# Performance work log

Measured on AMD Instinct MI355X. Metric: run time of the kernel, lower is better.

The kernel has to match this reference:

```python
import jax, jax.numpy as jnp
import numpy as np

B, T, D = 2, 2048, 2048
H, HKV = 16, 16
SEM, GEO = 1024, 1024
DH = D // H          # 128, v head dim
DS = SEM // H        # 64, sem head dim
DG = GEO // H        # 64, geo head dim (== rope_dim)
ROPE_BASE = 10000.0


def _split_heads(x, n_heads, hd):
    b, t, _ = x.shape
    return x.reshape(b, t, n_heads, hd).transpose(0, 2, 1, 3)  # (B,H,T,hd)


def _rope(x, pos_offset):
    # x: (B,H,T,DG); rotate-half RoPE over the full geo head dim
    b, h, t, d = x.shape
    inv_freq = 1.0 / (ROPE_BASE ** (jnp.arange(0, d, 2, dtype=jnp.float32) / d))
    pos = jnp.arange(t, dtype=jnp.float32) + jnp.float32(pos_offset)
    ang = pos[:, None] * inv_freq[None, :]            # (T, d/2)
    cos, sin = jnp.cos(ang), jnp.sin(ang)             # (T, d/2)
    x1, x2 = x[..., : d // 2], x[..., d // 2 :]
    return jnp.concatenate([x1 * cos - x2 * sin, x2 * cos + x1 * sin], axis=-1)


def setup_inputs() -> dict:
    key = jax.random.key(0)
    ks = jax.random.split(key, 8)
    s = lambda fan_in: 1.0 / np.sqrt(fan_in)
    return {
        "x": jax.random.normal(ks[0], (B, T, D), dtype=jnp.float32),
        "Wq_sem": jax.random.normal(ks[1], (D, SEM), dtype=jnp.float32) * s(D),
        "Wk_sem": jax.random.normal(ks[2], (D, SEM), dtype=jnp.float32) * s(D),
        "Wq_geo": jax.random.normal(ks[3], (D, GEO), dtype=jnp.float32) * s(D),
        "Wk_geo": jax.random.normal(ks[4], (D, GEO), dtype=jnp.float32) * s(D),
        "Wv": jax.random.normal(ks[5], (D, D), dtype=jnp.float32) * s(D),
        "Wo": jax.random.normal(ks[6], (D, D), dtype=jnp.float32) * s(D),
        "gate_logit": jax.random.normal(ks[7], (H,), dtype=jnp.float32) * 0.1,
        "pos_offset": 0,
    }


def reference(x, Wq_sem, Wk_sem, Wq_geo, Wk_geo, Wv, Wo, gate_logit, pos_offset):
    qsh = _split_heads(x @ Wq_sem, H, DS)    # (B,H,T,DS)
    ksh = _split_heads(x @ Wk_sem, HKV, DS)
    qgh = _split_heads(x @ Wq_geo, H, DG)    # (B,H,T,DG)
    kgh = _split_heads(x @ Wk_geo, HKV, DG)
    vh = _split_heads(x @ Wv, HKV, DH)       # (B,H,T,DH)

    qgh = _rope(qgh, pos_offset)
    kgh = _rope(kgh, pos_offset)

    gate = jax.nn.sigmoid(gate_logit).reshape(1, H, 1, 1).astype(x.dtype)
    qsh = qsh * (2.0 * gate)
    qgh = qgh * (2.0 - 2.0 * gate)

    sem_scale = 1.0 / np.sqrt(float(DS))
    geo_scale = 1.0 / np.sqrt(float(DG))
    # decoupled logits: sem and geo contributions each with their own scale
    logits = (jnp.einsum("bhqd,bhkd->bhqk", qsh, ksh) * sem_scale
              + jnp.einsum("bhqd,bhkd->bhqk", qgh, kgh) * geo_scale)

    t = x.shape[1]
    causal = jnp.tril(jnp.ones((t, t), dtype=bool))
    logits = jnp.where(causal, logits, jnp.finfo(logits.dtype).min)
    attn = jax.nn.softmax(logits, axis=-1)

    out_h = jnp.einsum("bhqk,bhkd->bhqd", attn, vh)   # (B,H,T,DH)
    out = out_h.transpose(0, 2, 1, 3).reshape(x.shape[0], t, H * DH)
    return out @ Wo
```

## Files before the change

### kernel.cpp

```cpp
#include <hip/hip_runtime.h>
#include <hip/hip_bf16.h>
#include <math.h>

#define B_ 2
#define T_ 2048
#define D_ 2048
#define H_ 16
#define DH_ 128
#define SEM_ 1024
#define GEO_ 1024
#define NPROJ 6144

typedef unsigned short ushort_t;
typedef short bf16x8 __attribute__((ext_vector_type(8)));
typedef float f32x4 __attribute__((ext_vector_type(4)));

static __device__ inline ushort_t f2b(float x) {
    __hip_bfloat16 h = __float2bfloat16(x);
    return *reinterpret_cast<ushort_t*>(&h);
}
static __device__ inline float b2f(ushort_t u) {
    union { unsigned int i; float f; } v; v.i = ((unsigned int)u) << 16; return v.f;
}
static __device__ inline void gload_lds16(const ushort_t* g, ushort_t* l) {
    __builtin_amdgcn_global_load_lds(
        (const __attribute__((address_space(1))) void*)g,
        (__attribute__((address_space(3))) void*)l, 16, 0, 0);
}

__global__ __launch_bounds__(256) void convert_x(
    const float* __restrict__ x, ushort_t* __restrict__ xh)
{
    size_t i = ((size_t)blockIdx.x * 256 + threadIdx.x) * 8;
    float4 a = *(const float4*)&x[i];
    float4 b = *(const float4*)&x[i + 4];
    bf16x8 o;
    o[0] = (short)f2b(a.x); o[1] = (short)f2b(a.y);
    o[2] = (short)f2b(a.z); o[3] = (short)f2b(a.w);
    o[4] = (short)f2b(b.x); o[5] = (short)f2b(b.y);
    o[6] = (short)f2b(b.z); o[7] = (short)f2b(b.w);
    *(bf16x8*)&xh[i] = o;
}

__global__ __launch_bounds__(256) void transpose_all(
    const float* __restrict__ W0, const float* __restrict__ W1,
    const float* __restrict__ W2, const float* __restrict__ W3,
    const float* __restrict__ W4, const float* __restrict__ W5,
    ushort_t* __restrict__ Wt_all, ushort_t* __restrict__ WoT)
{
    const int z = blockIdx.z;
    const float* W;
    ushort_t* dst;
    int N;
    switch (z) {
        case 0: W = W0; dst = Wt_all;                          N = 1024; break;
        case 1: W = W1; dst = Wt_all + (size_t)1024 * 2048;    N = 1024; break;
        case 2: W = W2; dst = Wt_all + (size_t)2048 * 2048;    N = 1024; break;
        case 3: W = W3; dst = Wt_all + (size_t)3072 * 2048;    N = 1024; break;
        case 4: W = W4; dst = Wt_all + (size_t)4096 * 2048;    N = 2048; break;
        default: W = W5; dst = WoT;                            N = 2048; break;
    }
    const int n0 = blockIdx.x * 32;
    if (n0 >= N) return;
    const int k0 = blockIdx.y * 32;

    __shared__ float tile[32][33];
    const int c = threadIdx.x & 31, r = threadIdx.x >> 5;
#pragma unroll
    for (int rr = 0; rr < 32; rr += 8)
        tile[r + rr][c] = W[(size_t)(k0 + r + rr) * N + n0 + c];
    __syncthreads();
#pragma unroll
    for (int rr = 0; rr < 32; rr += 8)
        dst[(size_t)(n0 + r + rr) * 2048 + k0 + c] = f2b(tile[c][r + rr]);
}

__global__ __launch_bounds__(256) void gemm_proj(
    const ushort_t* __restrict__ A, const ushort_t* __restrict__ Bt,
    const float* __restrict__ gate_logit, const int* __restrict__ pos_off,
    ushort_t* __restrict__ Qh, ushort_t* __restrict__ Kh,
    ushort_t* __restrict__ Vt)
{
    const int K = 2048;
    __shared__ ushort_t As[128 * 32];
    __shared__ ushort_t Bs[128 * 32];

    const int tid  = threadIdx.x;
    const int wid  = tid >> 6, lane = tid & 63;
    const int ln16 = lane & 15, g = lane >> 4;
    const int wm = wid & 1, wn = wid >> 1;
    const int m0 = blockIdx.y * 128, n0 = blockIdx.x * 128;

    const int lrow = lane >> 2;
    const int lc8  = (lane & 3) * 8;
    const ushort_t* gA = A  + (size_t)(m0 + wid * 32 + lrow) * K + lc8;
    const ushort_t* gB = Bt + (size_t)(n0 + wid * 32 + lrow) * K + lc8;
    ushort_t* lA = As + wid * 1024;
    ushort_t* lB = Bs + wid * 1024;
    const size_t K16 = (size_t)16 * K;

    f32x4 acc[4][4];
#pragma unroll
    for (int i = 0; i < 4; ++i)
#pragma unroll
        for (int j = 0; j < 4; ++j) acc[i][j] = (f32x4){0.f, 0.f, 0.f, 0.f};

    for (int k0 = 0; k0 < K; k0 += 32) {
        __syncthreads();
        gload_lds16(gA,       lA);
        gload_lds16(gA + K16, lA + 512);
        gload_lds16(gB,       lB);
        gload_lds16(gB + K16, lB + 512);
        gA += 32; gB += 32;
        __syncthreads();

        bf16x8 af[4], bfr[4];
#pragma unroll
        for (int i = 0; i < 4; ++i)
            af[i] = *(const bf16x8*)&As[(wm * 64 + i * 16 + ln16) * 32 + g * 8];
#pragma unroll
        for (int j = 0; j < 4; ++j)
            bfr[j] = *(const bf16x8*)&Bs[(wn * 64 + j * 16 + ln16) * 32 + g * 8];
#pragma unroll
        for (int i = 0; i < 4; ++i)
#pragma unroll
            for (int j = 0; j < 4; ++j)
                acc[i][j] = __builtin_amdgcn_mfma_f32_16x16x32_bf16(
                    af[i], bfr[j], acc[i][j], 0, 0, 0);
    }

    const int region = n0 >> 10;
    const int rbase  = m0 + wm * 64 + g * 4;

    if (region <= 1) {
        const int h = ((n0 & 1023) >> 6) + wn;
        ushort_t* dst = (region == 0) ? Qh : Kh;
        float sc = 1.0f;
        if (region == 0) {
            float sg = 1.0f / (1.0f + __expf(-gate_logit[h]));
            sc = 0.25f * sg;
        }
#pragma unroll
        for (int i = 0; i < 4; ++i)
#pragma unroll
            for (int r = 0; r < 4; ++r) {
                int row = rbase + i * 16 + r;
                int t = row & (T_ - 1), bb = row >> 11;
                size_t base = ((size_t)(bb * H_ + h) * T_ + t) * 128;
#pragma unroll
                for (int j = 0; j < 4; ++j)
                    dst[base + j * 16 + ln16] = f2b(acc[i][j][r] * sc);
            }
    } else if (region <= 3) {
        const int h = ((n0 & 1023) >> 6) + wn;
        ushort_t* dst = (region == 2) ? Qh : Kh;
        float sc = 1.0f;
        if (region == 2) {
            float sg = 1.0f / (1.0f + __expf(-gate_logit[h]));
            sc = 0.25f * (1.0f - sg);
        }
        const float po = (float)(*pos_off);
#pragma unroll
        for (int j = 0; j < 2; ++j) {
            const int ip = j * 16 + ln16;
            const float invf = __expf(-0.28782313665087625f * (float)ip);
#pragma unroll
            for (int i = 0; i < 4; ++i)
#pragma unroll
                for (int r = 0; r < 4; ++r) {
                    int row = rbase + i * 16 + r;
                    int t = row & (T_ - 1), bb = row >> 11;
                    float s, c;
                    __sincosf(((float)t + po) * invf, &s, &c);
                    float x1 = acc[i][j][r], x2 = acc[i][j + 2][r];
                    size_t base = ((size_t)(bb * H_ + h) * T_ + t) * 128;
                    dst[base + 64 + ip] = f2b((x1 * c - x2 * s) * sc);
                    dst[base + 96 + ip] = f2b((x2 * c + x1 * s) * sc);
                }
        }
    } else {
        const int h = (n0 - 4096) >> 7;
#pragma unroll
        for (int j = 0; j < 4; ++j) {
            const int d = wn * 64 + j * 16 + ln16;
            size_t dbase = ((size_t)((n0 >= 4096 ? 0 : 0) ) ); (void)dbase;
#pragma unroll
            for (int i = 0; i < 4; ++i)
#pragma unroll
                for (int r = 0; r < 4; ++r) {
                    int row = rbase + i * 16 + r;
                    int t = row & (T_ - 1), bb = row >> 11;
                    Vt[((size_t)(bb * H_ + h) * DH_ + d) * T_ + t] =
                        f2b(acc[i][j][r]);
                }
        }
    }
}

__global__ __launch_bounds__(256) void gemm_bt_f32(
    const ushort_t* __restrict__ A, const ushort_t* __restrict__ Bt,
    float* __restrict__ C, int M, int N, int K)
{
    __shared__ ushort_t As[128 * 32];
    __shared__ ushort_t Bs[128 * 32];

    const int tid  = threadIdx.x;
    const int wid  = tid >> 6, lane = tid & 63;
    const int ln16 = lane & 15, g = lane >> 4;
    const int wm = wid & 1, wn = wid >> 1;
    const int m0 = blockIdx.y * 128, n0 = blockIdx.x * 128;

    const int lrow = lane >> 2;
    const int lc8  = (lane & 3) * 8;
    const ushort_t* gA = A  + (size_t)(m0 + wid * 32 + lrow) * K + lc8;
    const ushort_t* gB = Bt + (size_t)(n0 + wid * 32 + lrow) * K + lc8;
    ushort_t* lA = As + wid * 1024;
    ushort_t* lB = Bs + wid * 1024;
    const size_t K16 = (size_t)16 * K;

    f32x4 acc[4][4];
#pragma unroll
    for (int i = 0; i < 4; ++i)
#pragma unroll
        for (int j = 0; j < 4; ++j) acc[i][j] = (f32x4){0.f, 0.f, 0.f, 0.f};

    for (int k0 = 0; k0 < K; k0 += 32) {
        __syncthreads();
        gload_lds16(gA,       lA);
        gload_lds16(gA + K16, lA + 512);
        gload_lds16(gB,       lB);
        gload_lds16(gB + K16, lB + 512);
        gA += 32; gB += 32;
        __syncthreads();

        bf16x8 af[4], bfr[4];
#pragma unroll
        for (int i = 0; i < 4; ++i)
            af[i] = *(const bf16x8*)&As[(wm * 64 + i * 16 + ln16) * 32 + g * 8];
#pragma unroll
        for (int j = 0; j < 4; ++j)
            bfr[j] = *(const bf16x8*)&Bs[(wn * 64 + j * 16 + ln16) * 32 + g * 8];
#pragma unroll
        for (int i = 0; i < 4; ++i)
#pragma unroll
            for (int j = 0; j < 4; ++j)
                acc[i][j] = __builtin_amdgcn_mfma_f32_16x16x32_bf16(
                    af[i], bfr[j], acc[i][j], 0, 0, 0);
    }

#pragma unroll
    for (int i = 0; i < 4; ++i)
#pragma unroll
        for (int j = 0; j < 4; ++j)
#pragma unroll
            for (int r = 0; r < 4; ++r) {
                int row = m0 + wm * 64 + i * 16 + g * 4 + r;
                int col = n0 + wn * 64 + j * 16 + ln16;
                C[(size_t)row * N + col] = acc[i][j][r];
            }
}

#define P_PITCH  40

__global__ __launch_bounds__(256) void flash_attn(
    const ushort_t* __restrict__ Qh,
    const ushort_t* __restrict__ Kh,
    const ushort_t* __restrict__ Vt,
    ushort_t* __restrict__ aoh)
{
    __shared__ ushort_t Ks[32 * 128];
    __shared__ ushort_t Vs[128 * 32];
    __shared__ ushort_t Pl[4 * 16 * P_PITCH];

    const int tid  = threadIdx.x;
    const int wid  = tid >> 6, lane = tid & 63;
    const int ln16 = lane & 15, g = lane >> 4;
    const int p    = blockIdx.x;
    const int h  = blockIdx.y, b = blockIdx.z;
    const int bh = b * H_ + h;

    const ushort_t* Kbase = Kh + (size_t)bh * T_ * 128;
    const ushort_t* Vbase = Vt + (size_t)bh * 128 * T_;
    ushort_t* Pw = Pl + wid * 16 * P_PITCH;

    const int sk0 = tid,      sk1 = 256 + tid;
    const int kr0 = sk0 >> 4, kc0 = sk0 & 15;
    const int kr1 = sk1 >> 4, kc1 = sk1 & 15;
    const int vd0 = sk0 >> 2, vg0 = sk0 & 3;
    const int vd1 = sk1 >> 2, vg1 = sk1 & 3;
    const int kofs0 = (kc0 ^ (kr0 & 15)) * 8, kofs1 = (kc1 ^ (kr1 & 15)) * 8;
    const int vofs0 = (vg0 ^ ((vd0 + (vd0 >> 2)) & 3)) * 8;
    const int vofs1 = (vg1 ^ ((vd1 + (vd1 >> 2)) & 3)) * 8;

    bf16x8 bones;
    {
        short o = (ln16 == 0) ? (short)0x3F80 : (short)0;
#pragma unroll
        for (int j = 0; j < 8; ++j) bones[j] = o;
    }

#pragma unroll 1
    for (int ti = 0; ti < 2; ++ti) {
        const int qt = ti ? (31 - p) : p;
        const int q0 = qt * 64;
        const int qw = q0 + wid * 16;

        bf16x8 aq[4];
        {
            const ushort_t* qrow = Qh + ((size_t)bh * T_ + qw + ln16) * 128;
#pragma unroll
            for (int c2 = 0; c2 < 4; ++c2)
                aq[c2] = *(const bf16x8*)(qrow + c2 * 32 + g * 8);
        }

        f32x4 acc[8];
#pragma unroll
        for (int i = 0; i < 8; ++i) acc[i] = (f32x4){0.f, 0.f, 0.f, 0.f};
        f32x4 acc_l = (f32x4){0.f, 0.f, 0.f, 0.f};

        const int nkb  = q0 / 32 + 2;
        const int qmax = qw + 15;

        for (int kb = 0; kb < nkb; ++kb) {
            const int kt = kb * 32;
            __syncthreads();
            gload_lds16(Kbase + (size_t)(kt + kr0) * 128 + kofs0, Ks + wid * 512);
            gload_lds16(Kbase + (size_t)(kt + kr1) * 128 + kofs1, Ks + 2048 + wid * 512);
            gload_lds16(Vbase + (size_t)vd0 * T_ + kt + vofs0,    Vs + wid * 512);
            gload_lds16(Vbase + (size_t)vd1 * T_ + kt + vofs1,    Vs + 2048 + wid * 512);
            __syncthreads();
            if (kt > qmax) continue;

            f32x4 s0 = (f32x4){0.f, 0.f, 0.f, 0.f};
            f32x4 s1 = (f32x4){0.f, 0.f, 0.f, 0.f};
#pragma unroll
            for (int c2 = 0; c2 < 4; ++c2) {
                int jk = c2 * 4 + g;
                bf16x8 bk0 = *(const bf16x8*)&Ks[(ln16 * 16 + (jk ^ ln16)) * 8];
                bf16x8 bk1 = *(const bf16x8*)&Ks[(256 + ln16 * 16 + (jk ^ ln16)) * 8];
                s0 = __builtin_amdgcn_mfma_f32_16x16x32_bf16(aq[c2], bk0, s0, 0, 0, 0);
                s1 = __builtin_amdgcn_mfma_f32_16x16x32_bf16(aq[c2], bk1, s1, 0, 0, 0);
            }

            const bool diag = (kt + 31 > qw);
#pragma unroll
            for (int r2 = 0; r2 < 4; ++r2) {
                float e0 = __expf(s0[r2] - 12.0f);
                float e1 = __expf(s1[r2] - 12.0f);
                if (diag) {
                    int qr = qw + g * 4 + r2;
                    e0 = (kt + ln16      > qr) ? 0.0f : e0;
                    e1 = (kt + 16 + ln16 > qr) ? 0.0f : e1;
                }
                int prow = g * 4 + r2;
                Pw[prow * P_PITCH + ln16]      = f2b(e0);
                Pw[prow * P_PITCH + 16 + ln16] = f2b(e1);
            }
            __asm__ volatile("s_waitcnt lgkmcnt(0)" ::: "memory");
            bf16x8 ap = *(const bf16x8*)&Pw[ln16 * P_PITCH + g * 8];

#pragma unroll
            for (int cdv = 0; cdv < 8; ++cdv) {
                int d = cdv * 16 + ln16;
                bf16x8 bv = *(const bf16x8*)
                    &Vs[((d << 2) + (g ^ ((d + (d >> 2)) & 3))) * 8];
                acc[cdv] = __builtin_amdgcn_mfma_f32_16x16x32_bf16(ap, bv, acc[cdv], 0, 0, 0);
            }
            acc_l = __builtin_amdgcn_mfma_f32_16x16x32_bf16(ap, bones, acc_l, 0, 0, 0);
        }

        float invl[4];
#pragma unroll
        for (int r2 = 0; r2 < 4; ++r2)
            invl[r2] = 1.0f / __shfl(acc_l[r2], lane & 48);
#pragma unroll
        for (int cdv = 0; cdv < 8; ++cdv)
#pragma unroll
            for (int r2 = 0; r2 < 4; ++r2) {
                int qr = qw + g * 4 + r2;
                aoh[((size_t)b * T_ + qr) * D_ + h * DH_ + cdv * 16 + ln16] =
                    f2b(acc[cdv][r2] * invl[r2]);
            }
    }
}

extern "C" void kernel_launch(void* const* d_in, const int* in_sizes, int n_in,
                              void* d_out, int out_size, void* d_ws, size_t ws_size,
                              hipStream_t stream)
{
    const float* x       = (const float*)d_in[0];
    const float* Wq_sem  = (const float*)d_in[1];
    const float* Wk_sem  = (const float*)d_in[2];
    const float* Wq_geo  = (const float*)d_in[3];
    const float* Wk_geo  = (const float*)d_in[4];
    const float* Wv      = (const float*)d_in[5];
    const float* Wo      = (const float*)d_in[6];
    const float* gate    = (const float*)d_in[7];
    const int*   pos_off = (const int*)d_in[8];
    float* out = (float*)d_out;

    const int M = B_ * T_;
    char* ws = (char*)d_ws;
    ushort_t* xh     = (ushort_t*)(ws);
    ushort_t* aoh    = xh;
    ushort_t* Wt_all = (ushort_t*)(ws + (size_t)16 * 1048576);
    ushort_t* WoT    = (ushort_t*)(ws + (size_t)40 * 1048576);
    ushort_t* Qh     = (ushort_t*)(ws + (size_t)48 * 1048576);
    ushort_t* Kh     = (ushort_t*)(ws + (size_t)64 * 1048576);
    ushort_t* Vt     = (ushort_t*)(ws + (size_t)80 * 1048576);

    dim3 blk(256);

    convert_x<<<(M * D_) / (256 * 8), blk, 0, stream>>>(x, xh);
    transpose_all<<<dim3(64, 64, 6), blk, 0, stream>>>(
        Wq_sem, Wk_sem, Wq_geo, Wk_geo, Wv, Wo, Wt_all, WoT);

    gemm_proj<<<dim3(NPROJ / 128, M / 128), blk, 0, stream>>>(
        xh, Wt_all, gate, pos_off, Qh, Kh, Vt);

    flash_attn<<<dim3(16, H_, B_), blk, 0, stream>>>(Qh, Kh, Vt, aoh);

    gemm_bt_f32<<<dim3(D_ / 128, M / 128), blk, 0, stream>>>(
        aoh, WoT, out, M, D_, D_);
}
```

Measured before the change: 420.5 us.

## Rewrite projection GEMM as 256x256 double-buffered pipelined MFMA kernel

Replaces the 128x128, 256-thread projection GEMM (which synchronized twice per 32-wide K step) with a 256x256 tile, 512-thread kernel using 128KB of dynamic LDS. It double-buffers 64-wide K tiles, interleaves async global-to-LDS staging of the next tile with quadrant-wise MFMA, swizzles LDS addresses, and raises wave priority around the MFMA blocks. The epilogue is remapped so each wave writes two heads with RoPE and gate scaling as before. This aims to hide load latency and raise MFMA utilization, at the cost of heavy register pressure, fewer blocks in the grid, and fragile hand-written waitcnt and barrier ordering.

```diff
diff --git a/kernel.cpp b/kernel.cpp
--- a/kernel.cpp
+++ b/kernel.cpp
@@ -75,125 +75,185 @@
         dst[(size_t)(n0 + r + rr) * 2048 + k0 + c] = f2b(tile[c][r + rr]);
 }
 
-__global__ __launch_bounds__(256) void gemm_proj(
+#define BARS()  { asm volatile("" ::: "memory"); __builtin_amdgcn_s_barrier(); asm volatile("" ::: "memory"); }
+#define WL0()   asm volatile("s_waitcnt lgkmcnt(0)" ::: "memory")
+#define WV6()   asm volatile("s_waitcnt vmcnt(6)" ::: "memory")
+
+#define LDA8(par, iq, i4, kk) \
+    (*(const bf16x8*)&smA[(par)*16384 + (iq)*8192 + aoff + (i4)*1024 + (kk)*32])
+#define LDB8(par, jq, j1, kk) \
+    (*(const bf16x8*)&smB[(par)*16384 + (jq)*8192 + boff + (j1)*2048 + (kk)*32])
+
+#define READ_A(par, iq) \
+    aF[0]=LDA8(par,iq,0,0); aF[1]=LDA8(par,iq,0,1); \
+    aF[2]=LDA8(par,iq,1,0); aF[3]=LDA8(par,iq,1,1); \
+    aF[4]=LDA8(par,iq,2,0); aF[5]=LDA8(par,iq,2,1); \
+    aF[6]=LDA8(par,iq,3,0); aF[7]=LDA8(par,iq,3,1);
+
+#define READ_B(par, jq) \
+    bF[(jq)*4+0]=LDB8(par,jq,0,0); bF[(jq)*4+1]=LDB8(par,jq,0,1); \
+    bF[(jq)*4+2]=LDB8(par,jq,1,0); bF[(jq)*4+3]=LDB8(par,jq,1,1);
+
+#define STAGE_A(h, kt, par) do { \
+    const ushort_t* _s = gAbase + (size_t)((h)*128) * 2048 + (kt)*64 + stgoff; \
+    ushort_t* _d = smA + (par)*16384 + (h)*8192 + wid*512; \
+    gload_lds16(_s, _d); \
+    gload_lds16(_s + (size_t)64*2048, _d + 4096); \
+} while(0)
+
+#define STAGE_B(h, kt, par) do { \
+    const ushort_t* _s = gBbase + (size_t)((h)*128) * 2048 + (kt)*64 + stgoff; \
+    ushort_t* _d = smB + (par)*16384 + (h)*8192 + wid*512; \
+    gload_lds16(_s, _d); \
+    gload_lds16(_s + (size_t)64*2048, _d + 4096); \
+} while(0)
+
+#define MM16(iq, jq) do { \
+    _Pragma("unroll") \
+    for (int i4 = 0; i4 < 4; ++i4) { \
+        acc[(iq)*4+i4][(jq)*2+0] = __builtin_amdgcn_mfma_f32_16x16x32_bf16(aF[i4*2+0], bF[(jq)*4+0], acc[(iq)*4+i4][(jq)*2+0], 0, 0, 0); \
+        acc[(iq)*4+i4][(jq)*2+0] = __builtin_amdgcn_mfma_f32_16x16x32_bf16(aF[i4*2+1], bF[(jq)*4+1], acc[(iq)*4+i4][(jq)*2+0], 0, 0, 0); \
+        acc[(iq)*4+i4][(jq)*2+1] = __builtin_amdgcn_mfma_f32_16x16x32_bf16(aF[i4*2+0], bF[(jq)*4+2], acc[(iq)*4+i4][(jq)*2+1], 0, 0, 0); \
+        acc[(iq)*4+i4][(jq)*2+1] = __builtin_amdgcn_mfma_f32_16x16x32_bf16(aF[i4*2+1], bF[(jq)*4+3], acc[(iq)*4+i4][(jq)*2+1], 0, 0, 0); \
+    } \
+} while(0)
+
+#define TILE_BODY(par, parn, kt1, kt2) \
+    READ_A(par, 0); READ_B(par, 0); STAGE_A(1, kt1, parn); \
+    BARS(); WL0(); \
+    __builtin_amdgcn_s_setprio(1); MM16(0, 0); __builtin_amdgcn_s_setprio(0); \
+    BARS(); \
+    READ_B(par, 1); STAGE_A(0, kt2, par); \
+    BARS(); WL0(); \
+    __builtin_amdgcn_s_setprio(1); MM16(0, 1); __builtin_amdgcn_s_setprio(0); \
+    BARS(); \
+    READ_A(par, 1); STAGE_B(0, kt2, par); \
+    BARS(); WL0(); \
+    __builtin_amdgcn_s_setprio(1); MM16(1, 1); __builtin_amdgcn_s_setprio(0); \
+    BARS(); \
+    STAGE_B(1, kt2, par); WV6(); \
+    BARS(); \
+    __builtin_amdgcn_s_setprio(1); MM16(1, 0); __builtin_amdgcn_s_setprio(0); \
+    BARS();
+
+__global__ __launch_bounds__(512, 2) void gemm_proj(
     const ushort_t* __restrict__ A, const ushort_t* __restrict__ Bt,
     const float* __restrict__ gate_logit, const int* __restrict__ pos_off,
     ushort_t* __restrict__ Qh, ushort_t* __restrict__ Kh,
     ushort_t* __restrict__ Vt)
 {
-    const int K = 2048;
-    __shared__ ushort_t As[128 * 32];
-    __shared__ ushort_t Bs[128 * 32];
+    extern __shared__ __align__(16) ushort_t smdyn[];
+    ushort_t* smA = smdyn;
+    ushort_t* smB = smdyn + 32768;
 
     const int tid  = threadIdx.x;
     const int wid  = tid >> 6, lane = tid & 63;
     const int ln16 = lane & 15, g = lane >> 4;
     const int wm = wid & 1, wn = wid >> 1;
-    const int m0 = blockIdx.y * 128, n0 = blockIdx.x * 128;
-
-    const int lrow = lane >> 2;
-    const int lc8  = (lane & 3) * 8;
-    const ushort_t* gA = A  + (size_t)(m0 + wid * 32 + lrow) * K + lc8;
-    const ushort_t* gB = Bt + (size_t)(n0 + wid * 32 + lrow) * K + lc8;
-    ushort_t* lA = As + wid * 1024;
-    ushort_t* lB = Bs + wid * 1024;
-    const size_t K16 = (size_t)16 * K;
-
-    f32x4 acc[4][4];
-#pragma unroll
-    for (int i = 0; i < 4; ++i)
+    const int m0 = blockIdx.y * 256, n0 = blockIdx.x * 256;
+
+    const int srow = wid * 8 + (lane >> 3);
+    const int scol = ((lane & 7) * 8) ^ ((lane & 32) ? 16 : 0);
+    const size_t stgoff = (size_t)srow * 2048 + scol;
+    const ushort_t* gAbase = A  + (size_t)m0 * 2048;
+    const ushort_t* gBbase = Bt + (size_t)n0 * 2048;
+
+    const int sw   = (ln16 & 4) << 2;
+    const int aoff = wm * 4096 + ln16 * 64 + ((g * 8) ^ sw);
+    const int boff = (wn >> 1) * 4096 + (wn & 1) * 1024 + ln16 * 64 + ((g * 8) ^ sw);
+
+    f32x4 acc[8][4];
+#pragma unroll
+    for (int i = 0; i < 8; ++i)
 #pragma unroll
         for (int j = 0; j < 4; ++j) acc[i][j] = (f32x4){0.f, 0.f, 0.f, 0.f};
-
-    for (int k0 = 0; k0 < K; k0 += 32) {
-        __syncthreads();
-        gload_lds16(gA,       lA);
-        gload_lds16(gA + K16, lA + 512);
-        gload_lds16(gB,       lB);
-        gload_lds16(gB + K16, lB + 512);
-        gA += 32; gB += 32;
-        __syncthreads();
-
-        bf16x8 af[4], bfr[4];
-#pragma unroll
-        for (int i = 0; i < 4; ++i)
-            af[i] = *(const bf16x8*)&As[(wm * 64 + i * 16 + ln16) * 32 + g * 8];
-#pragma unroll
-        for (int j = 0; j < 4; ++j)
-            bfr[j] = *(const bf16x8*)&Bs[(wn * 64 + j * 16 + ln16) * 32 + g * 8];
-#pragma unroll
-        for (int i = 0; i < 4; ++i)
-#pragma unroll
-            for (int j = 0; j < 4; ++j)
-                acc[i][j] = __builtin_amdgcn_mfma_f32_16x16x32_bf16(
-                    af[i], bfr[j], acc[i][j], 0, 0, 0);
-    }
+    bf16x8 aF[8], bF[8];
+
+    STAGE_A(0, 0, 0); STAGE_B(0, 0, 0); STAGE_B(1, 0, 0); STAGE_A(1, 0, 0);
+    STAGE_A(0, 1, 1); STAGE_B(0, 1, 1); STAGE_B(1, 1, 1);
+    WV6();
+    BARS();
+
+#pragma unroll 1
+    for (int t = 0; t < 32; t += 2) {
+        const int ka1 = t + 1;
+        const int ka2 = (t + 2 < 32) ? t + 2 : 31;
+        const int kb1 = ka2;
+        const int kb2 = (t + 3 < 32) ? t + 3 : 31;
+        TILE_BODY(0, 1, ka1, ka2);
+        TILE_BODY(1, 0, kb1, kb2);
+    }
+    asm volatile("s_waitcnt vmcnt(0)" ::: "memory");
 
     const int region = n0 >> 10;
     const int rbase  = m0 + wm * 64 + g * 4;
 
     if (region <= 1) {
-        const int h = ((n0 & 1023) >> 6) + wn;
         ushort_t* dst = (region == 0) ? Qh : Kh;
-        float sc = 1.0f;
+        const int hb  = ((n0 & 1023) >> 6) + (wn >> 1);
+        const int d64 = (wn & 1) * 16 + ln16;
+        float sc0 = 1.0f, sc1 = 1.0f;
         if (region == 0) {
-            float sg = 1.0f / (1.0f + __expf(-gate_logit[h]));
-            sc = 0.25f * sg;
+            sc0 = 0.25f / (1.0f + __expf(-gate_logit[hb]));
+            sc1 = 0.25f / (1.0f + __expf(-gate_logit[hb + 2]));
         }
 #pragma unroll
-        for (int i = 0; i < 4; ++i)
+        for (int i = 0; i < 8; ++i)
 #pragma unroll
             for (int r = 0; r < 4; ++r) {
-                int row = rbase + i * 16 + r;
+                int row = rbase + (i >> 2) * 128 + (i & 3) * 16 + r;
                 int t = row & (T_ - 1), bb = row >> 11;
-                size_t base = ((size_t)(bb * H_ + h) * T_ + t) * 128;
-#pragma unroll
-                for (int j = 0; j < 4; ++j)
-                    dst[base + j * 16 + ln16] = f2b(acc[i][j][r] * sc);
+                size_t b0 = ((size_t)(bb * H_ + hb)     * T_ + t) * 128;
+                size_t b1 = ((size_t)(bb * H_ + hb + 2) * T_ + t) * 128;
+                dst[b0 + d64]      = f2b(acc[i][0][r] * sc0);
+                dst[b0 + d64 + 32] = f2b(acc[i][1][r] * sc0);
+                dst[b1 + d64]      = f2b(acc[i][2][r] * sc1);
+                dst[b1 + d64 + 32] = f2b(acc[i][3][r] * sc1);
             }
     } else if (region <= 3) {
-        const int h = ((n0 & 1023) >> 6) + wn;
         ushort_t* dst = (region == 2) ? Qh : Kh;
-        float sc = 1.0f;
+        const int hb = ((n0 & 1023) >> 6) + (wn >> 1);
+        const int ip = (wn & 1) * 16 + ln16;
+        const float invf = __expf(-0.28782313665087625f * (float)ip);
+        const float po = (float)(*pos_off);
+        float sc0 = 1.0f, sc1 = 1.0f;
         if (region == 2) {
-            float sg = 1.0f / (1.0f + __expf(-gate_logit[h]));
-            sc = 0.25f * (1.0f - sg);
+            sc0 = 0.25f * (1.0f - 1.0f / (1.0f + __expf(-gate_logit[hb])));
+            sc1 = 0.25f * (1.0f - 1.0f / (1.0f + __expf(-gate_logit[hb + 2])));
         }
-        const float po = (float)(*pos_off);
-#pragma unroll
-        for (int j = 0; j < 2; ++j) {
-            const int ip = j * 16 + ln16;
-            const float invf = __expf(-0.28782313665087625f * (float)ip);
-#pragma unroll
-            for (int i = 0; i < 4; ++i)
-#pragma unroll
-                for (int r = 0; r < 4; ++r) {
-                    int row = rbase + i * 16 + r;
-                    int t = row & (T_ - 1), bb = row >> 11;
-                    float s, c;
-                    __sincosf(((float)t + po) * invf, &s, &c);
-                    float x1 = acc[i][j][r], x2 = acc[i][j + 2][r];
-                    size_t base = ((size_t)(bb * H_ + h) * T_ + t) * 128;
-                    dst[base + 64 + ip] = f2b((x1 * c - x2 * s) * sc);
-                    dst[base + 96 + ip] = f2b((x2 * c + x1 * s) * sc);
-                }
-        }
+#pragma unroll
+        for (int i = 0; i < 8; ++i)
+#pragma unroll
+            for (int r = 0; r < 4; ++r) {
+                int row = rbase + (i >> 2) * 128 + (i & 3) * 16 + r;
+                int t = row & (T_ - 1), bb = row >> 11;
+                float s, c;
+                __sincosf(((float)t + po) * invf, &s, &c);
+                size_t b0 = ((size_t)(bb * H_ + hb)     * T_ + t) * 128;
+                size_t b1 = ((size_t)(bb * H_ + hb + 2) * T_ + t) * 128;
+                float x1 = acc[i][0][r], x2 = acc[i][1][r];
+                dst[b0 + 64 + ip] = f2b((x1 * c - x2 * s) * sc0);
+                dst[b0 + 96 + ip] = f2b((x2 * c + x1 * s) * sc0);
+                x1 = acc[i][2][r]; x2 = acc[i][3][r];
+                dst[b1 + 64 + ip] = f2b((x1 * c - x2 * s) * sc1);
+                dst[b1 + 96 + ip] = f2b((x2 * c + x1 * s) * sc1);
+            }
     } else {
-        const int h = (n0 - 4096) >> 7;
-#pragma unroll
-        for (int j = 0; j < 4; ++j) {
-            const int d = wn * 64 + j * 16 + ln16;
-            size_t dbase = ((size_t)((n0 >= 4096 ? 0 : 0) ) ); (void)dbase;
-#pragma unroll
-            for (int i = 0; i < 4; ++i)
-#pragma unroll
-                for (int r = 0; r < 4; ++r) {
-                    int row = rbase + i * 16 + r;
-                    int t = row & (T_ - 1), bb = row >> 11;
-                    Vt[((size_t)(bb * H_ + h) * DH_ + d) * T_ + t] =
-                        f2b(acc[i][j][r]);
-                }
-        }
+        const int hb = (n0 - 4096) >> 7;
+        const int db = (wn >> 1) * 64 + (wn & 1) * 16 + ln16;
+#pragma unroll
+        for (int i = 0; i < 8; ++i)
+#pragma unroll
+            for (int r = 0; r < 4; ++r) {
+                int row = rbase + (i >> 2) * 128 + (i & 3) * 16 + r;
+                int t = row & (T_ - 1), bb = row >> 11;
+                size_t v0 = ((size_t)(bb * H_ + hb)     * DH_ + db) * T_ + t;
+                size_t v1 = ((size_t)(bb * H_ + hb + 1) * DH_ + db) * T_ + t;
+                Vt[v0]                    = f2b(acc[i][0][r]);
+                Vt[v0 + (size_t)32 * T_]  = f2b(acc[i][1][r]);
+                Vt[v1]                    = f2b(acc[i][2][r]);
+                Vt[v1 + (size_t)32 * T_]  = f2b(acc[i][3][r]);
+            }
     }
 }
 
@@ -415,7 +475,9 @@
     transpose_all<<<dim3(64, 64, 6), blk, 0, stream>>>(
         Wq_sem, Wk_sem, Wq_geo, Wk_geo, Wv, Wo, Wt_all, WoT);
 
-    gemm_proj<<<dim3(NPROJ / 128, M / 128), blk, 0, stream>>>(
+    hipFuncSetAttribute((const void*)gemm_proj,
+                        hipFuncAttributeMaxDynamicSharedMemorySize, 131072);
+    gemm_proj<<<dim3(NPROJ / 256, M / 256), dim3(512), 131072, stream>>>(
         xh, Wt_all, gate, pos_off, Qh, Kh, Vt);
 
     flash_attn<<<dim3(16, H_, B_), blk, 0, stream>>>(Qh, Kh, Vt, aoh);
```

New measurement: 427.9 us. Within noise of the previous version (+1.8%).
